# Performance work log

Measured on AMD Instinct MI355X. Metric: run time of the kernel, lower is better.

## Reference

```python
import jax, jax.numpy as jnp
import numpy as np

H, KVH, DH = 32, 8, 128        # attention heads, kv heads, head dim (shared by both streams)
G = H // KVH                   # GQA group size
EPS = 1e-6


def rms_norm(x, w):
    xf = x.astype(jnp.float32)
    n = xf * jax.lax.rsqrt(jnp.mean(xf * xf, axis=-1, keepdims=True) + EPS)
    return (n * w).astype(x.dtype)


def apply_rope(x, positions, max_wavelength=10000.0):
    # x: [B, L, h, DH], positions: [B, L]
    d_half = x.shape[-1] // 2
    freq_exponents = (2.0 / x.shape[-1]) * jnp.arange(d_half, dtype=jnp.float32)
    timescale = max_wavelength ** freq_exponents
    radians = positions[..., None].astype(jnp.float32) / timescale          # [B, L, d_half]
    radians = radians[..., None, :]                                         # [B, L, 1, d_half]
    s, c = jnp.sin(radians), jnp.cos(radians)
    xf = x.astype(jnp.float32)
    x1, x2 = xf[..., :d_half], xf[..., d_half:]
    out = jnp.concatenate([x1 * c - x2 * s, x2 * c + x1 * s], axis=-1)
    return out.astype(x.dtype)


def setup_inputs() -> dict:
    key = jax.random.key(0)
    ks = jax.random.split(key, 16)
    B, LV, LE = 2, 1024, 64
    DV, DE = 2560, 1920
    s = 0.02
    inp = {
        "vlm_embeds": jax.random.normal(ks[0], (B, LV, DV), jnp.float32),
        "expert_embeds": jax.random.normal(ks[1], (B, LE, DE), jnp.float32),
        "position_ids": jnp.sort(jax.random.randint(ks[2], (B, LV + LE), 0, 2048), axis=-1),
        "attention_mask": jnp.ones((B, LV + LE, LV + LE), dtype=bool),
        "w_ln_vlm": jnp.ones((DV,), jnp.float32),
        "Wq_vlm": jax.random.normal(ks[3], (DV, H * DH), jnp.float32) * s,
        "Wk_vlm": jax.random.normal(ks[4], (DV, KVH * DH), jnp.float32) * s,
        "Wv_vlm": jax.random.normal(ks[5], (DV, KVH * DH), jnp.float32) * s,
        "Wo_vlm": jax.random.normal(ks[6], (H * DH, DV), jnp.float32) * s,
        "w_ln_exp": jnp.ones((DE,), jnp.float32),
        "Wq_exp": jax.random.normal(ks[7], (DE, H * DH), jnp.float32) * s,
        "Wk_exp": jax.random.normal(ks[8], (DE, KVH * DH), jnp.float32) * s,
        "Wv_exp": jax.random.normal(ks[9], (DE, KVH * DH), jnp.float32) * s,
        "Wo_exp": jax.random.normal(ks[10], (H * DH, DE), jnp.float32) * s,
    }
    return inp


def _mixed_attn_layer(vlm_embeds, expert_embeds,
                      w_ln_vlm, Wq_vlm, Wk_vlm, Wv_vlm, Wo_vlm,
                      w_ln_exp, Wq_exp, Wk_exp, Wv_exp, Wo_exp,
                      position_ids, attention_mask, knowledge_insulation=True):
    B, LV, _ = vlm_embeds.shape
    LE = expert_embeds.shape[1]

    # Stream 0: VLM prefix (knowledge insulation -> no grad into VLM path).
    hv = rms_norm(vlm_embeds, w_ln_vlm)
    qv = (hv @ Wq_vlm).reshape(B, LV, H, DH)
    kv = (hv @ Wk_vlm).reshape(B, LV, KVH, DH)
    vv = (hv @ Wv_vlm).reshape(B, LV, KVH, DH)
    if knowledge_insulation:
        qv = jax.lax.stop_gradient(qv)
        kv = jax.lax.stop_gradient(kv)
        vv = jax.lax.stop_gradient(vv)

    # Stream 1: expert suffix.
    he = rms_norm(expert_embeds, w_ln_exp)
    qe = (he @ Wq_exp).reshape(B, LE, H, DH)
    ke = (he @ Wk_exp).reshape(B, LE, KVH, DH)
    ve = (he @ Wv_exp).reshape(B, LE, KVH, DH)

    # Concatenate streams along the sequence dim, then inline RoPE on q and k.
    q = jnp.concatenate([qv, qe], axis=1)          # [B, L, 32, 128]
    k = jnp.concatenate([kv, ke], axis=1)          # [B, L, 8, 128]
    v = jnp.concatenate([vv, ve], axis=1)
    q = apply_rope(q, position_ids)
    k = apply_rope(k, position_ids)

    # Eager GQA attention in fp32 (matches _eager_attention_forward).
    k_full = jnp.repeat(k, G, axis=2)              # kv-head major, group minor
    v_full = jnp.repeat(v, G, axis=2)
    att = jnp.einsum("bqhd,bkhd->bhqk", q.astype(jnp.float32), k_full.astype(jnp.float32))
    att = att * (DH ** -0.5)
    big_neg = jnp.finfo(jnp.float32).min
    att = jnp.where(attention_mask[:, None, :, :], att, big_neg)
    probs = jax.nn.softmax(att, axis=-1).astype(v_full.dtype)
    out = jnp.einsum("bhqk,bkhd->bqhd", probs, v_full).reshape(B, LV + LE, H * DH)

    # Split back to streams, per-stream output projection + residual.
    out_vlm = vlm_embeds + out[:, :LV] @ Wo_vlm
    out_exp = expert_embeds + out[:, LV:] @ Wo_exp
    return out_vlm, out_exp


def reference(vlm_embeds, expert_embeds, position_ids, attention_mask,
              w_ln_vlm, Wq_vlm, Wk_vlm, Wv_vlm, Wo_vlm,
              w_ln_exp, Wq_exp, Wk_exp, Wv_exp, Wo_exp):
    _, out_exp = _mixed_attn_layer(
        vlm_embeds, expert_embeds,
        w_ln_vlm, Wq_vlm, Wk_vlm, Wv_vlm, Wo_vlm,
        w_ln_exp, Wq_exp, Wk_exp, Wv_exp, Wo_exp,
        position_ids, attention_mask)
    return out_exp
```

## Files before the change

### kernel.cpp

```cpp
#include <hip/hip_runtime.h>
#include <hip/hip_bf16.h>
#include <cstddef>

#define B_  2
#define LV_ 1024
#define LE_ 64
#define S_TOT 1088
#define DV_ 2560
#define DE_ 1920
#define H_  32
#define KVH_ 8
#define DH_ 128
#define HD_ 4096
#define KVD_ 1024
#define NSPL 9

typedef short short8 __attribute__((ext_vector_type(8)));
typedef float f32x4 __attribute__((ext_vector_type(4)));

typedef __hip_bfloat16 bf16;

__device__ inline float b2f(bf16 h) { return __bfloat162float(h); }
__device__ inline bf16 f2b(float f) { return __float2bfloat16(f); }

typedef const __attribute__((address_space(1))) void* gptr_t;
typedef __attribute__((address_space(3))) void* lptr_t;
__device__ inline void gl16(const void* g, void* l) {
  __builtin_amdgcn_global_load_lds((gptr_t)g, (lptr_t)l, 16, 0, 0);
}

#define OFF_HVB   0ul
#define OFF_WKVT  10485760ul
#define OFF_HEB   20971520ul
#define OFF_WQKVT 21463040ul
#define OFF_QE    45056000ul
#define OFF_KBUF  46104576ul
#define OFF_VBUF  50561024ul
#define OFF_AO    59473920ul
#define OFF_M     20971520ul
#define OFF_L     21118976ul
#define OFF_OP    21463040ul
#define OFF_P2    21463040ul

#define NSPLIT2 16

__global__ __launch_bounds__(256) void rmsnorm_both(
    const float* __restrict__ xv, const float* __restrict__ wv,
    bf16* __restrict__ ov,
    const float* __restrict__ xe, const float* __restrict__ we,
    bf16* __restrict__ oe) {
  int row; const float* x; const float* w; bf16* o; int D;
  if (blockIdx.x < 2048) { row = blockIdx.x;        x = xv; w = wv; o = ov; D = DV_; }
  else                   { row = blockIdx.x - 2048; x = xe; w = we; o = oe; D = DE_; }
  const float4* x4 = (const float4*)(x + (size_t)row * D);
  const float4* w4 = (const float4*)w;
  int D4 = D >> 2;
  float ss = 0.f;
  for (int i = threadIdx.x; i < D4; i += 256) {
    float4 v = x4[i];
    ss += v.x * v.x + v.y * v.y + v.z * v.z + v.w * v.w;
  }
  __shared__ float red[256];
  red[threadIdx.x] = ss; __syncthreads();
  for (int s = 128; s > 0; s >>= 1) {
    if (threadIdx.x < s) red[threadIdx.x] += red[threadIdx.x + s];
    __syncthreads();
  }
  float inv = rsqrtf(red[0] / (float)D + 1e-6f);
  ushort4* o4 = (ushort4*)(o + (size_t)row * D);
  for (int i = threadIdx.x; i < D4; i += 256) {
    float4 v = x4[i], wv2 = w4[i];
    bf16 a = f2b(v.x * inv * wv2.x), b = f2b(v.y * inv * wv2.y);
    bf16 c = f2b(v.z * inv * wv2.z), d = f2b(v.w * inv * wv2.w);
    ushort4 ow;
    ow.x = *(ushort*)&a; ow.y = *(ushort*)&b; ow.z = *(ushort*)&c; ow.w = *(ushort*)&d;
    o4[i] = ow;
  }
}

__device__ inline void tile_tconv(float (*t)[65],
    const float* __restrict__ W, bf16* __restrict__ Wt,
    int K, int N, int n_off, int bx, int by) {
  int n0 = bx * 64, k0 = by * 64;
  int tid = threadIdx.x;
  int c = tid & 63, r4 = tid >> 6;
#pragma unroll 4
  for (int it = 0; it < 16; ++it) {
    int k = it * 4 + r4;
    t[k][c] = W[(size_t)(k0 + k) * N + n0 + c];
  }
  __syncthreads();
#pragma unroll 4
  for (int it = 0; it < 16; ++it) {
    int n = it * 4 + r4;
    Wt[(size_t)(n_off + n0 + n) * K + k0 + c] = f2b(t[c][n]);
  }
}

__global__ __launch_bounds__(256) void tconv_all(
    const float* __restrict__ Wk_vlm, const float* __restrict__ Wv_vlm,
    const float* __restrict__ Wq_exp, const float* __restrict__ Wk_exp,
    const float* __restrict__ Wv_exp,
    bf16* __restrict__ WkvT, bf16* __restrict__ WqkvT) {
  __shared__ float t[64][65];
  int id = blockIdx.x;
  if (id < 640)       tile_tconv(t, Wk_vlm, WkvT, DV_, KVD_, 0,    id % 16, id / 16);
  else if (id < 1280) { id -= 640;  tile_tconv(t, Wv_vlm, WkvT,  DV_, KVD_, 1024, id % 16, id / 16); }
  else if (id < 3200) { id -= 1280; tile_tconv(t, Wq_exp, WqkvT, DE_, HD_,  0,    id % 64, id / 64); }
  else if (id < 3680) { id -= 3200; tile_tconv(t, Wk_exp, WqkvT, DE_, KVD_, 4096, id % 16, id / 16); }
  else                { id -= 3680; tile_tconv(t, Wv_exp, WqkvT, DE_, KVD_, 5120, id % 16, id / 16); }
}

__global__ __launch_bounds__(256) void gemm_fused(
    const bf16* __restrict__ hv, const bf16* __restrict__ WkvT,
    const bf16* __restrict__ he, const bf16* __restrict__ WqkvT,
    bf16* __restrict__ kbuf, bf16* __restrict__ vbuf, bf16* __restrict__ qe) {
  __shared__ ushort As[4][64][32];
  __shared__ ushort Bs[4][128][32];
  int tid = threadIdx.x;
  int lane = tid & 63, w = tid >> 6;
  int lr = lane & 15, quad = lane >> 4;
  int wmA = (w >> 1) * 32, wnB = (w & 1) * 64;

  bool expert = (blockIdx.x >= 512);
  const ushort* Ab; const ushort* Bb; int K, nsteps, m0, n0;
  if (!expert) {
    m0 = (int)(blockIdx.x >> 4) * 64; n0 = (int)(blockIdx.x & 15) * 128;
    Ab = (const ushort*)hv; Bb = (const ushort*)WkvT;
    K = DV_; nsteps = DV_ / 32;
  } else {
    int e = (int)blockIdx.x - 512;
    m0 = (e / 48) * 64; n0 = (e % 48) * 128;
    Ab = (const ushort*)he; Bb = (const ushort*)WqkvT;
    K = DE_; nsteps = DE_ / 32;
  }

  int rA  = w * 16 + (lane >> 2);
  int rB0 = w * 32 + (lane >> 2);
  int rB1 = rB0 + 16;
  int sA  = (lane & 3) ^ ((rA  >> 1) & 3);
  int sB0 = (lane & 3) ^ ((rB0 >> 1) & 3);
  int sB1 = (lane & 3) ^ ((rB1 >> 1) & 3);
  const ushort* pa  = Ab + (size_t)(m0 + rA)  * K + sA  * 8;
  const ushort* pb0 = Bb + (size_t)(n0 + rB0) * K + sB0 * 8;
  const ushort* pb1 = Bb + (size_t)(n0 + rB1) * K + sB1 * 8;

  auto STAGE = [&](int buf, int t) {
    int k0 = t * 32;
    gl16(pa  + k0, &As[buf][w * 16][0]);
    gl16(pb0 + k0, &Bs[buf][w * 32][0]);
    gl16(pb1 + k0, &Bs[buf][w * 32 + 16][0]);
  };

  int sslot = (quad ^ ((lr >> 1) & 3)) * 8;

  f32x4 acc[2][4] = {};

  STAGE(0, 0);
  STAGE(1, 1);
  STAGE(2, 2);
  for (int t = 0; t < nsteps; ++t) {
    int rem = nsteps - t;
    if (rem > 3) {
      STAGE((t + 3) & 3, t + 3);
      asm volatile("s_waitcnt vmcnt(9)" ::: "memory");
    } else if (rem == 3) {
      asm volatile("s_waitcnt vmcnt(6)" ::: "memory");
    } else if (rem == 2) {
      asm volatile("s_waitcnt vmcnt(3)" ::: "memory");
    } else {
      asm volatile("s_waitcnt vmcnt(0)" ::: "memory");
    }
    __builtin_amdgcn_s_barrier();

    int cur = t & 3;
    short8 af[2], bv[4];
#pragma unroll
    for (int i = 0; i < 2; ++i)
      af[i] = *(const short8*)&As[cur][wmA + i * 16 + lr][sslot];
#pragma unroll
    for (int j = 0; j < 4; ++j)
      bv[j] = *(const short8*)&Bs[cur][wnB + j * 16 + lr][sslot];
    __builtin_amdgcn_s_setprio(1);
#pragma unroll
    for (int i = 0; i < 2; ++i)
#pragma unroll
      for (int j = 0; j < 4; ++j)
        acc[i][j] = __builtin_amdgcn_mfma_f32_16x16x32_bf16(af[i], bv[j], acc[i][j], 0, 0, 0);
    __builtin_amdgcn_s_setprio(0);

    __builtin_amdgcn_s_barrier();
  }

#pragma unroll
  for (int i = 0; i < 2; ++i) {
    int mm_base = wmA + i * 16 + quad * 4;
#pragma unroll
    for (int j = 0; j < 4; ++j) {
      int gn = n0 + wnB + j * 16 + lr;
#pragma unroll
      for (int r = 0; r < 4; ++r) {
        int mm = mm_base + r;
        float v = acc[i][j][r];
        if (!expert) {
          int m = m0 + mm;
          int b = m >> 10, s = m & 1023;
          size_t row = (size_t)(b * S_TOT + s);
          if (gn < 1024) kbuf[row * KVD_ + gn] = f2b(v);
          else           vbuf[row * KVD_ + (gn - 1024)] = f2b(v);
        } else {
          int m = m0 + mm;
          int b = m >> 6, l = m & 63;
          if (gn < 4096) {
            qe[(size_t)m * HD_ + gn] = f2b(v);
          } else {
            size_t row = (size_t)(b * S_TOT + LV_ + l);
            if (gn < 5120) kbuf[row * KVD_ + (gn - 4096)] = f2b(v);
            else           vbuf[row * KVD_ + (gn - 5120)] = f2b(v);
          }
        }
      }
    }
  }
}

__global__ __launch_bounds__(256) void gemm_out(
    const bf16* __restrict__ A, const float* __restrict__ W,
    float* __restrict__ partial) {
  __shared__ ushort As[128][40];
  __shared__ ushort Bs[64][40];
  int tid = threadIdx.x;
  int lane = tid & 63, wid = tid >> 6;
  int wm = (wid >> 1) * 64, wn = (wid & 1) * 32;
  int n0 = blockIdx.x * 64;
  int k_beg = blockIdx.y * 256;
  int lr = lane & 15, quad = lane >> 4;

  f32x4 acc[4][2] = {};

  int ar = tid >> 2;
  int ac = (tid & 3) * 8;
  const ushort* Aptr = (const ushort*)A + (size_t)ar * HD_ + ac;
  int bn = tid & 63, kg = tid >> 6;
  int bslot_w = ((kg ^ (bn & 3)) * 8);
  int brd = (quad ^ (lr & 3)) * 8;

  for (int k0 = k_beg; k0 < k_beg + 256; k0 += 32) {
    short8 a0 = *(const short8*)(Aptr + k0);
    short8 a1 = *(const short8*)(Aptr + (size_t)64 * HD_ + k0);
    float wv[8];
#pragma unroll
    for (int j = 0; j < 8; ++j)
      wv[j] = W[(size_t)(k0 + kg * 8 + j) * DE_ + n0 + bn];
    short8 bvv;
#pragma unroll
    for (int j = 0; j < 8; ++j) { bf16 h = f2b(wv[j]); bvv[j] = *(short*)&h; }
    __syncthreads();
    *(short8*)&As[ar][ac] = a0;
    *(short8*)&As[64 + ar][ac] = a1;
    *(short8*)&Bs[bn][bslot_w] = bvv;
    __syncthreads();
    short8 af[4], bfr[2];
#pragma unroll
    for (int i = 0; i < 4; ++i)
      af[i]  = *(const short8*)&As[wm + i * 16 + lr][quad * 8];
#pragma unroll
    for (int j = 0; j < 2; ++j)
      bfr[j] = *(const short8*)&Bs[wn + j * 16 + lr][brd];
#pragma unroll
    for (int i = 0; i < 4; ++i)
#pragma unroll
      for (int j = 0; j < 2; ++j)
        acc[i][j] = __builtin_amdgcn_mfma_f32_16x16x32_bf16(af[i], bfr[j], acc[i][j], 0, 0, 0);
  }

  float* pbase = partial + (size_t)blockIdx.y * 128 * 1920;
#pragma unroll
  for (int i = 0; i < 4; ++i) {
    int m_base = wm + i * 16 + quad * 4;
#pragma unroll
    for (int j = 0; j < 2; ++j) {
      int gn = n0 + wn + j * 16 + lr;
#pragma unroll
      for (int r = 0; r < 4; ++r)
        pbase[(size_t)(m_base + r) * 1920 + gn] = acc[i][j][r];
    }
  }
}

__global__ __launch_bounds__(256) void reduce_out(
    const float* __restrict__ partial, const float* __restrict__ residual,
    float* __restrict__ out) {
  int idx = (blockIdx.x * 256 + threadIdx.x) * 4;
  f32x4 s = *(const f32x4*)(residual + idx);
#pragma unroll
  for (int sp = 0; sp < NSPLIT2; ++sp) {
    const f32x4 v = *(const f32x4*)(partial + (size_t)sp * 128 * 1920 + idx);
    s += v;
  }
  *(f32x4*)(out + idx) = s;
}

__global__ __launch_bounds__(256) void rope_fused(
    bf16* __restrict__ qe, bf16* __restrict__ kbuf,
    const int* __restrict__ pos_ids) {
  if (blockIdx.x < 128) {
    int row = blockIdx.x;
    int b = row >> 6, l = row & 63;
    float pos = (float)pos_ids[b * S_TOT + LV_ + l];
    bf16* qrow = qe + (size_t)row * HD_;
    for (int p = threadIdx.x; p < H_ * 64; p += 256) {
      int hh = p >> 6, i = p & 63;
      float inv_ts = expf(-9.210340371976184f * (float)i * (1.0f / 64.0f));
      float r = pos * inv_ts;
      float sn = sinf(r), cs = cosf(r);
      float x1 = b2f(qrow[hh * DH_ + i]), x2 = b2f(qrow[hh * DH_ + i + 64]);
      qrow[hh * DH_ + i]      = f2b(x1 * cs - x2 * sn);
      qrow[hh * DH_ + i + 64] = f2b(x2 * cs + x1 * sn);
    }
  } else {
    int bid = blockIdx.x - 128;
    int s = bid % S_TOT, b = bid / S_TOT;
    float pos = (float)pos_ids[b * S_TOT + s];
    size_t base = ((size_t)(b * S_TOT + s)) * KVD_;
    for (int t = threadIdx.x; t < KVH_ * 64; t += 256) {
      int kvh = t >> 6, i = t & 63;
      size_t idx = base + kvh * DH_ + i;
      float inv_ts = expf(-9.210340371976184f * (float)i * (1.0f / 64.0f));
      float r = pos * inv_ts;
      float sn = sinf(r), cs = cosf(r);
      float x1 = b2f(kbuf[idx]), x2 = b2f(kbuf[idx + 64]);
      kbuf[idx]      = f2b(x1 * cs - x2 * sn);
      kbuf[idx + 64] = f2b(x2 * cs + x1 * sn);
    }
  }
}

__global__ __launch_bounds__(256) void attn_part(
    const bf16* __restrict__ qe, const bf16* __restrict__ kbuf,
    const bf16* __restrict__ vbuf,
    float* __restrict__ O_p, float* __restrict__ m_arr,
    float* __restrict__ l_arr) {
  int bh = blockIdx.x & 63;
  int split = blockIdx.x >> 6;
  int h = bh & 31, b = bh >> 5;
  int kvh = h >> 2;
  int tid = threadIdx.x;
  int lane = tid & 63, wid = tid >> 6;
  int lr = lane & 15, quad = lane >> 4;

  __shared__ ushort Ks[64][152];
  __shared__ ushort vTs[128][72];
  __shared__ ushort sc[4][16][72];

  short8 qf[4];
  {
    const ushort* qptr = (const ushort*)qe +
        ((size_t)(b * LE_ + wid * 16 + lr)) * HD_ + h * DH_ + quad * 8;
#pragma unroll
    for (int ks = 0; ks < 4; ++ks) qf[ks] = *(const short8*)(qptr + ks * 32);
  }

  f32x4 Of[8] = {};
  float m_i[4], l_i[4];
#pragma unroll
  for (int r = 0; r < 4; ++r) { m_i[r] = -1e30f; l_i[r] = 0.f; }

  const float scale = 0.08838834764831845f;
  int nch = (split == 8) ? 1 : 2;

  for (int c = 0; c < nch; ++c) {
    int key0 = split * 128 + c * 64;
    __syncthreads();
    {
      int dg = tid & 15, kq = tid >> 4;
#pragma unroll
      for (int it = 0; it < 4; ++it) {
        int key = it * 16 + kq;
        short8 v = *(const short8*)((const ushort*)kbuf +
            ((size_t)(b * S_TOT + key0 + key) * KVH_ + kvh) * DH_ + dg * 8);
        *(short8*)&Ks[key][dg * 8] = v;
      }
    }
    {
      int key = tid & 63, dgrp = tid >> 6;
      const ushort* vp = (const ushort*)vbuf +
          ((size_t)(b * S_TOT + key0 + key) * KVH_ + kvh) * DH_ + dgrp * 32;
      short8 vv[4];
#pragma unroll
      for (int q8 = 0; q8 < 4; ++q8) vv[q8] = *(const short8*)(vp + q8 * 8);
#pragma unroll
      for (int q8 = 0; q8 < 4; ++q8)
#pragma unroll
        for (int j = 0; j < 8; ++j)
          vTs[dgrp * 32 + q8 * 8 + j][key] = (ushort)vv[q8][j];
    }
    __syncthreads();

    f32x4 Sf[4] = {};
#pragma unroll
    for (int kt = 0; kt < 4; ++kt)
#pragma unroll
      for (int ks = 0; ks < 4; ++ks) {
        short8 kf = *(const short8*)&Ks[kt * 16 + lr][quad * 8 + ks * 32];
        Sf[kt] = __builtin_amdgcn_mfma_f32_16x16x32_bf16(qf[ks], kf, Sf[kt], 0, 0, 0);
      }

#pragma unroll
    for (int kt = 0; kt < 4; ++kt) Sf[kt] *= scale;
#pragma unroll
    for (int r = 0; r < 4; ++r) {
      float mx = fmaxf(fmaxf(Sf[0][r], Sf[1][r]), fmaxf(Sf[2][r], Sf[3][r]));
#pragma unroll
      for (int msk = 1; msk < 16; msk <<= 1) mx = fmaxf(mx, __shfl_xor(mx, msk));
      float mn = fmaxf(m_i[r], mx);
      float alpha = __expf(m_i[r] - mn);
      m_i[r] = mn;
      float ls = 0.f;
#pragma unroll
      for (int kt = 0; kt < 4; ++kt) {
        float p = __expf(Sf[kt][r] - mn);
        Sf[kt][r] = p;
        ls += p;
      }
      l_i[r] = l_i[r] * alpha + ls;
#pragma unroll
      for (int nt = 0; nt < 8; ++nt) Of[nt][r] *= alpha;
#pragma unroll
      for (int kt = 0; kt < 4; ++kt) {
        bf16 t = f2b(Sf[kt][r]);
        sc[wid][quad * 4 + r][kt * 16 + lr] = *(ushort*)&t;
      }
    }

#pragma unroll
    for (int ks = 0; ks < 2; ++ks) {
      short8 pf = *(const short8*)&sc[wid][lr][quad * 8 + ks * 32];
#pragma unroll
      for (int nt = 0; nt < 8; ++nt) {
        short8 vf = *(const short8*)&vTs[nt * 16 + lr][quad * 8 + ks * 32];
        Of[nt] = __builtin_amdgcn_mfma_f32_16x16x32_bf16(pf, vf, Of[nt], 0, 0, 0);
      }
    }
  }

  float l_row[4];
#pragma unroll
  for (int r = 0; r < 4; ++r) {
    float l = l_i[r];
#pragma unroll
    for (int msk = 1; msk < 16; msk <<= 1) l += __shfl_xor(l, msk);
    l_row[r] = l;
  }

  size_t rbase = (size_t)split * 4096 + (size_t)bh * 64;
#pragma unroll
  for (int nt = 0; nt < 8; ++nt)
#pragma unroll
    for (int r = 0; r < 4; ++r) {
      int q = wid * 16 + quad * 4 + r;
      O_p[(rbase + q) * 128 + nt * 16 + lr] = Of[nt][r];
    }
  if (lr == 0) {
#pragma unroll
    for (int r = 0; r < 4; ++r) {
      int q = wid * 16 + quad * 4 + r;
      m_arr[rbase + q] = m_i[r];
      l_arr[rbase + q] = l_row[r];
    }
  }
}

__global__ __launch_bounds__(256) void attn_combine(
    const float* __restrict__ O_p, const float* __restrict__ m_arr,
    const float* __restrict__ l_arr, bf16* __restrict__ ao) {
  int t = blockIdx.x * 256 + threadIdx.x;
  int d = t & 127, row = t >> 7;
  float m_g = -1e30f;
#pragma unroll
  for (int s = 0; s < NSPL; ++s) m_g = fmaxf(m_g, m_arr[s * 4096 + row]);
  float denom = 0.f, acc = 0.f;
#pragma unroll
  for (int s = 0; s < NSPL; ++s) {
    float w = __expf(m_arr[s * 4096 + row] - m_g);
    denom += w * l_arr[s * 4096 + row];
    acc   += w * O_p[((size_t)s * 4096 + row) * 128 + d];
  }
  int b = row >> 11, h = (row >> 6) & 31, q = row & 63;
  bf16 o = f2b(acc / denom);
  ((ushort*)ao)[((size_t)(b * 64 + q) * 32 + h) * 128 + d] = *(ushort*)&o;
}

extern "C" void kernel_launch(void* const* d_in, const int* in_sizes, int n_in,
                              void* d_out, int out_size, void* d_ws, size_t ws_size,
                              hipStream_t stream) {
  const float* vlm      = (const float*)d_in[0];
  const float* expe     = (const float*)d_in[1];
  const int*   pos      = (const int*)d_in[2];
  const float* w_ln_vlm = (const float*)d_in[4];
  const float* Wk_vlm   = (const float*)d_in[6];
  const float* Wv_vlm   = (const float*)d_in[7];
  const float* w_ln_exp = (const float*)d_in[9];
  const float* Wq_exp   = (const float*)d_in[10];
  const float* Wk_exp   = (const float*)d_in[11];
  const float* Wv_exp   = (const float*)d_in[12];
  const float* Wo_exp   = (const float*)d_in[13];
  float* out = (float*)d_out;
  char* ws = (char*)d_ws;

  bf16* hv_b  = (bf16*)(ws + OFF_HVB);
  bf16* WkvT  = (bf16*)(ws + OFF_WKVT);
  bf16* he_b  = (bf16*)(ws + OFF_HEB);
  bf16* WqkvT = (bf16*)(ws + OFF_WQKVT);
  bf16* qe    = (bf16*)(ws + OFF_QE);
  bf16* kbuf  = (bf16*)(ws + OFF_KBUF);
  bf16* vbuf  = (bf16*)(ws + OFF_VBUF);
  bf16* ao    = (bf16*)(ws + OFF_AO);
  float* m_arr = (float*)(ws + OFF_M);
  float* l_arr = (float*)(ws + OFF_L);
  float* O_p   = (float*)(ws + OFF_OP);
  float* part2 = (float*)(ws + OFF_P2);

  rmsnorm_both<<<B_ * LV_ + B_ * LE_, 256, 0, stream>>>(
      vlm, w_ln_vlm, hv_b, expe, w_ln_exp, he_b);

  tconv_all<<<4160, 256, 0, stream>>>(Wk_vlm, Wv_vlm, Wq_exp, Wk_exp, Wv_exp,
                                      WkvT, WqkvT);

  gemm_fused<<<608, 256, 0, stream>>>(hv_b, WkvT, he_b, WqkvT, kbuf, vbuf, qe);

  rope_fused<<<128 + B_ * S_TOT, 256, 0, stream>>>(qe, kbuf, pos);

  attn_part<<<64 * NSPL, 256, 0, stream>>>(qe, kbuf, vbuf, O_p, m_arr, l_arr);
  attn_combine<<<4096 * 128 / 256, 256, 0, stream>>>(O_p, m_arr, l_arr, ao);

  gemm_out<<<dim3(30, NSPLIT2), 256, 0, stream>>>(ao, Wo_exp, part2);
  reduce_out<<<128 * 1920 / 4 / 256, 256, 0, stream>>>(part2, expe, out);
}
```

Before: 299.5 us.

## Double attention key splits and replace split-K reduce with atomic accumulation

Attention is now split into 17 chunks of 64 keys instead of 9 chunks of 128, so each block handles one chunk without an online-softmax loop and the grid roughly doubles. The output projection's split-K partials now go straight into the output with float atomicAdd, after a device-to-device copy seeds the output with the residual. This drops the reduce kernel and its partial buffer traffic. In exchange the combine step has more partials to merge, the atomics may contend, and float summation order becomes nondeterministic.

Result: slower. 306.5 us (+2.4%).

```diff
diff --git a/kernel.cpp b/kernel.cpp
--- a/kernel.cpp
+++ b/kernel.cpp
@@ -13,7 +13,7 @@
 #define DH_ 128
 #define HD_ 4096
 #define KVD_ 1024
-#define NSPL 9
+#define NSPL 17
 
 typedef short short8 __attribute__((ext_vector_type(8)));
 typedef float f32x4 __attribute__((ext_vector_type(4)));
@@ -37,12 +37,9 @@
 #define OFF_KBUF  46104576ul
 #define OFF_VBUF  50561024ul
 #define OFF_AO    59473920ul
-#define OFF_M     20971520ul
-#define OFF_L     21118976ul
-#define OFF_OP    21463040ul
-#define OFF_P2    21463040ul
-
-#define NSPLIT2 16
+#define OFF_OP    0ul
+#define OFF_M     35651584ul
+#define OFF_L     35930112ul
 
 __global__ __launch_bounds__(256) void rmsnorm_both(
     const float* __restrict__ xv, const float* __restrict__ wv,
@@ -226,7 +223,7 @@
 
 __global__ __launch_bounds__(256) void gemm_out(
     const bf16* __restrict__ A, const float* __restrict__ W,
-    float* __restrict__ partial) {
+    float* __restrict__ out) {
   __shared__ ushort As[128][40];
   __shared__ ushort Bs[64][40];
   int tid = threadIdx.x;
@@ -274,7 +271,6 @@
         acc[i][j] = __builtin_amdgcn_mfma_f32_16x16x32_bf16(af[i], bfr[j], acc[i][j], 0, 0, 0);
   }
 
-  float* pbase = partial + (size_t)blockIdx.y * 128 * 1920;
 #pragma unroll
   for (int i = 0; i < 4; ++i) {
     int m_base = wm + i * 16 + quad * 4;
@@ -283,22 +279,9 @@
       int gn = n0 + wn + j * 16 + lr;
 #pragma unroll
       for (int r = 0; r < 4; ++r)
-        pbase[(size_t)(m_base + r) * 1920 + gn] = acc[i][j][r];
-    }
-  }
-}
-
-__global__ __launch_bounds__(256) void reduce_out(
-    const float* __restrict__ partial, const float* __restrict__ residual,
-    float* __restrict__ out) {
-  int idx = (blockIdx.x * 256 + threadIdx.x) * 4;
-  f32x4 s = *(const f32x4*)(residual + idx);
-#pragma unroll
-  for (int sp = 0; sp < NSPLIT2; ++sp) {
-    const f32x4 v = *(const f32x4*)(partial + (size_t)sp * 128 * 1920 + idx);
-    s += v;
-  }
-  *(f32x4*)(out + idx) = s;
+        atomicAdd(&out[(size_t)(m_base + r) * 1920 + gn], acc[i][j][r]);
+    }
+  }
 }
 
 __global__ __launch_bounds__(256) void rope_fused(
@@ -363,84 +346,74 @@
 
   f32x4 Of[8] = {};
   float m_i[4], l_i[4];
-#pragma unroll
-  for (int r = 0; r < 4; ++r) { m_i[r] = -1e30f; l_i[r] = 0.f; }
 
   const float scale = 0.08838834764831845f;
-  int nch = (split == 8) ? 1 : 2;
-
-  for (int c = 0; c < nch; ++c) {
-    int key0 = split * 128 + c * 64;
-    __syncthreads();
-    {
-      int dg = tid & 15, kq = tid >> 4;
-#pragma unroll
-      for (int it = 0; it < 4; ++it) {
-        int key = it * 16 + kq;
-        short8 v = *(const short8*)((const ushort*)kbuf +
-            ((size_t)(b * S_TOT + key0 + key) * KVH_ + kvh) * DH_ + dg * 8);
-        *(short8*)&Ks[key][dg * 8] = v;
-      }
-    }
-    {
-      int key = tid & 63, dgrp = tid >> 6;
-      const ushort* vp = (const ushort*)vbuf +
-          ((size_t)(b * S_TOT + key0 + key) * KVH_ + kvh) * DH_ + dgrp * 32;
-      short8 vv[4];
-#pragma unroll
-      for (int q8 = 0; q8 < 4; ++q8) vv[q8] = *(const short8*)(vp + q8 * 8);
-#pragma unroll
-      for (int q8 = 0; q8 < 4; ++q8)
-#pragma unroll
-        for (int j = 0; j < 8; ++j)
-          vTs[dgrp * 32 + q8 * 8 + j][key] = (ushort)vv[q8][j];
-    }
-    __syncthreads();
-
-    f32x4 Sf[4] = {};
-#pragma unroll
-    for (int kt = 0; kt < 4; ++kt)
-#pragma unroll
-      for (int ks = 0; ks < 4; ++ks) {
-        short8 kf = *(const short8*)&Ks[kt * 16 + lr][quad * 8 + ks * 32];
-        Sf[kt] = __builtin_amdgcn_mfma_f32_16x16x32_bf16(qf[ks], kf, Sf[kt], 0, 0, 0);
-      }
-
-#pragma unroll
-    for (int kt = 0; kt < 4; ++kt) Sf[kt] *= scale;
-#pragma unroll
-    for (int r = 0; r < 4; ++r) {
-      float mx = fmaxf(fmaxf(Sf[0][r], Sf[1][r]), fmaxf(Sf[2][r], Sf[3][r]));
-#pragma unroll
-      for (int msk = 1; msk < 16; msk <<= 1) mx = fmaxf(mx, __shfl_xor(mx, msk));
-      float mn = fmaxf(m_i[r], mx);
-      float alpha = __expf(m_i[r] - mn);
-      m_i[r] = mn;
-      float ls = 0.f;
-#pragma unroll
-      for (int kt = 0; kt < 4; ++kt) {
-        float p = __expf(Sf[kt][r] - mn);
-        Sf[kt][r] = p;
-        ls += p;
-      }
-      l_i[r] = l_i[r] * alpha + ls;
-#pragma unroll
-      for (int nt = 0; nt < 8; ++nt) Of[nt][r] *= alpha;
-#pragma unroll
-      for (int kt = 0; kt < 4; ++kt) {
-        bf16 t = f2b(Sf[kt][r]);
-        sc[wid][quad * 4 + r][kt * 16 + lr] = *(ushort*)&t;
-      }
-    }
-
-#pragma unroll
-    for (int ks = 0; ks < 2; ++ks) {
-      short8 pf = *(const short8*)&sc[wid][lr][quad * 8 + ks * 32];
-#pragma unroll
-      for (int nt = 0; nt < 8; ++nt) {
-        short8 vf = *(const short8*)&vTs[nt * 16 + lr][quad * 8 + ks * 32];
-        Of[nt] = __builtin_amdgcn_mfma_f32_16x16x32_bf16(pf, vf, Of[nt], 0, 0, 0);
-      }
+  int key0 = split * 64;
+
+  {
+    int dg = tid & 15, kq = tid >> 4;
+#pragma unroll
+    for (int it = 0; it < 4; ++it) {
+      int key = it * 16 + kq;
+      short8 v = *(const short8*)((const ushort*)kbuf +
+          ((size_t)(b * S_TOT + key0 + key) * KVH_ + kvh) * DH_ + dg * 8);
+      *(short8*)&Ks[key][dg * 8] = v;
+    }
+  }
+  {
+    int key = tid & 63, dgrp = tid >> 6;
+    const ushort* vp = (const ushort*)vbuf +
+        ((size_t)(b * S_TOT + key0 + key) * KVH_ + kvh) * DH_ + dgrp * 32;
+    short8 vv[4];
+#pragma unroll
+    for (int q8 = 0; q8 < 4; ++q8) vv[q8] = *(const short8*)(vp + q8 * 8);
+#pragma unroll
+    for (int q8 = 0; q8 < 4; ++q8)
+#pragma unroll
+      for (int j = 0; j < 8; ++j)
+        vTs[dgrp * 32 + q8 * 8 + j][key] = (ushort)vv[q8][j];
+  }
+  __syncthreads();
+
+  f32x4 Sf[4] = {};
+#pragma unroll
+  for (int kt = 0; kt < 4; ++kt)
+#pragma unroll
+    for (int ks = 0; ks < 4; ++ks) {
+      short8 kf = *(const short8*)&Ks[kt * 16 + lr][quad * 8 + ks * 32];
+      Sf[kt] = __builtin_amdgcn_mfma_f32_16x16x32_bf16(qf[ks], kf, Sf[kt], 0, 0, 0);
+    }
+
+#pragma unroll
+  for (int kt = 0; kt < 4; ++kt) Sf[kt] *= scale;
+#pragma unroll
+  for (int r = 0; r < 4; ++r) {
+    float mx = fmaxf(fmaxf(Sf[0][r], Sf[1][r]), fmaxf(Sf[2][r], Sf[3][r]));
+#pragma unroll
+    for (int msk = 1; msk < 16; msk <<= 1) mx = fmaxf(mx, __shfl_xor(mx, msk));
+    m_i[r] = mx;
+    float ls = 0.f;
+#pragma unroll
+    for (int kt = 0; kt < 4; ++kt) {
+      float p = __expf(Sf[kt][r] - mx);
+      Sf[kt][r] = p;
+      ls += p;
+    }
+    l_i[r] = ls;
+#pragma unroll
+    for (int kt = 0; kt < 4; ++kt) {
+      bf16 t = f2b(Sf[kt][r]);
+      sc[wid][quad * 4 + r][kt * 16 + lr] = *(ushort*)&t;
+    }
+  }
+
+#pragma unroll
+  for (int ks = 0; ks < 2; ++ks) {
+    short8 pf = *(const short8*)&sc[wid][lr][quad * 8 + ks * 32];
+#pragma unroll
+    for (int nt = 0; nt < 8; ++nt) {
+      short8 vf = *(const short8*)&vTs[nt * 16 + lr][quad * 8 + ks * 32];
+      Of[nt] = __builtin_amdgcn_mfma_f32_16x16x32_bf16(pf, vf, Of[nt], 0, 0, 0);
     }
   }
 
@@ -516,10 +489,12 @@
   bf16* kbuf  = (bf16*)(ws + OFF_KBUF);
   bf16* vbuf  = (bf16*)(ws + OFF_VBUF);
   bf16* ao    = (bf16*)(ws + OFF_AO);
+  float* O_p   = (float*)(ws + OFF_OP);
   float* m_arr = (float*)(ws + OFF_M);
   float* l_arr = (float*)(ws + OFF_L);
-  float* O_p   = (float*)(ws + OFF_OP);
-  float* part2 = (float*)(ws + OFF_P2);
+
+  hipMemcpyAsync(out, expe, (size_t)B_ * LE_ * DE_ * sizeof(float),
+                 hipMemcpyDeviceToDevice, stream);
 
   rmsnorm_both<<<B_ * LV_ + B_ * LE_, 256, 0, stream>>>(
       vlm, w_ln_vlm, hv_b, expe, w_ln_exp, he_b);
@@ -534,6 +509,5 @@
   attn_part<<<64 * NSPL, 256, 0, stream>>>(qe, kbuf, vbuf, O_p, m_arr, l_arr);
   attn_combine<<<4096 * 128 / 256, 256, 0, stream>>>(O_p, m_arr, l_arr, ao);
 
-  gemm_out<<<dim3(30, NSPLIT2), 256, 0, stream>>>(ao, Wo_exp, part2);
-  reduce_out<<<128 * 1920 / 4 / 256, 256, 0, stream>>>(part2, expe, out);
-}
+  gemm_out<<<dim3(30, 16), 256, 0, stream>>>(ao, Wo_exp, out);
+}
```
